# Kernel tuning notes

Measured on AMD Instinct MI355X. Metric: run time of the kernel, lower is better.

The kernel has to match this reference:

```python
import jax, jax.numpy as jnp
import numpy as np

K = 9
VOCAB = 7
DIM = 512
LOW = 256  # downsampled bottleneck dim
N_LAYERS = 2
EPS = 1e-5


def _inorm(x, g, b):
    # InstanceNorm1d over length axis (biased var), x: (N, C, K)
    m = jnp.mean(x, axis=-1, keepdims=True)
    v = jnp.mean((x - m) ** 2, axis=-1, keepdims=True)
    return g[None, :, None] * (x - m) * jax.lax.rsqrt(v + EPS) + b[None, :, None]


def _conv5_same(x, w, b):
    # x: (N, C, K), w: (O, C, 5), dilation 1, padding 'same' -> pad 2
    y = jax.lax.conv_general_dilated(
        x, w, window_strides=(1,), padding=[(2, 2)],
        dimension_numbers=('NCH', 'OIH', 'NCH'))
    return y + b[None, :, None]


def _bytenet_layer(x, p):
    (g1, b1, g2, b2, g3, b3, w1, c1b, w2, c2b, w3, c3b) = p
    h = jax.nn.gelu(_inorm(x, g1, b1), approximate=False)
    h = jnp.einsum('nck,oc->nok', h, w1) + c1b[None, :, None]      # 1x1 conv 512->256
    h = jax.nn.gelu(_inorm(h, g2, b2), approximate=False)
    h = _conv5_same(h, w2, c2b)                                     # k=5 conv 256->256
    h = jax.nn.gelu(_inorm(h, g3, b3), approximate=False)
    h = jnp.einsum('nck,oc->nok', h, w3) + c3b[None, :, None]      # 1x1 conv 256->512
    return h + x  # dropout is identity in eval


def setup_inputs() -> dict:
    key = jax.random.key(0)
    ks = jax.random.split(key, 16)
    x = jax.random.randint(ks[0], (8, 2048), 0, VOCAB)
    emb = jax.random.normal(ks[1], (VOCAB, DIM), jnp.float32) * 0.02
    emb = emb.at[6].set(0.0)  # padding_idx=6
    d = {
        'x': x,
        'emb': emb,
        'ln1_w': jnp.ones((N_LAYERS, DIM)), 'ln1_b': jnp.zeros((N_LAYERS, DIM)),
        'ln2_w': jnp.ones((N_LAYERS, LOW)), 'ln2_b': jnp.zeros((N_LAYERS, LOW)),
        'ln3_w': jnp.ones((N_LAYERS, LOW)), 'ln3_b': jnp.zeros((N_LAYERS, LOW)),
        'c1_w': jax.random.normal(ks[2], (N_LAYERS, LOW, DIM), jnp.float32) * 0.02,
        'c1_b': jnp.zeros((N_LAYERS, LOW)),
        'c2_w': jax.random.normal(ks[3], (N_LAYERS, LOW, LOW, 5), jnp.float32) * 0.02,
        'c2_b': jnp.zeros((N_LAYERS, LOW)),
        'c3_w': jax.random.normal(ks[4], (N_LAYERS, DIM, LOW), jnp.float32) * 0.02,
        'c3_b': jnp.zeros((N_LAYERS, DIM)),
        'out_w': jax.random.normal(ks[5], (VOCAB, DIM * K), jnp.float32) * 0.02,
        'out_b': jnp.zeros((VOCAB,)),
    }
    return d


def reference(x, emb, ln1_w, ln1_b, ln2_w, ln2_b, ln3_w, ln3_b,
              c1_w, c1_b, c2_w, c2_b, c3_w, c3_b, out_w, out_b):
    B, L = x.shape
    W = L - K + 1
    e = emb[x]                                        # (B, L, D)
    idx = jnp.arange(W)[:, None] + jnp.arange(K)      # (W, K)
    win = e[:, idx, :]                                # (B, W, K, D)
    h = win.transpose(0, 1, 3, 2).reshape(B * W, DIM, K)  # (N, D, K)
    for i in range(N_LAYERS):
        p = (ln1_w[i], ln1_b[i], ln2_w[i], ln2_b[i], ln3_w[i], ln3_b[i],
             c1_w[i], c1_b[i], c2_w[i], c2_b[i], c3_w[i], c3_b[i])
        h = _bytenet_layer(h, p)
    pred = h.reshape(B * W, DIM * K) @ out_w.T + out_b
    return pred.reshape(B, W, VOCAB)
```

## Files before the change

### kernel.cpp

```cpp
#include <hip/hip_runtime.h>

typedef __attribute__((ext_vector_type(8))) short bfv8;
typedef __attribute__((ext_vector_type(4))) float f32x4;
typedef __attribute__((ext_vector_type(4))) unsigned short usv4;

typedef __attribute__((address_space(1))) const void gvoid;
typedef __attribute__((address_space(3))) void lvoid;
__device__ __forceinline__ void gload16(const void* g, void* l) {
  __builtin_amdgcn_global_load_lds((gvoid*)g, (lvoid*)l, 16, 0, 0);
}

__device__ __forceinline__ float bf2f(unsigned short u) {
  union { unsigned int i; float f; } c; c.i = ((unsigned int)u) << 16; return c.f;
}
__device__ __forceinline__ unsigned short f2bf(float f) {
  union { float f; unsigned int i; } c; c.f = f;
  unsigned int r = c.i + 0x7FFFu + ((c.i >> 16) & 1u);
  return (unsigned short)(r >> 16);
}
__device__ __forceinline__ float gelu_(float x) {
  float z2 = 1.5957691216057308f * x * __builtin_fmaf(0.044715f, x * x, 1.0f);
  float e = __expf(z2);
  float t = __builtin_amdgcn_rcpf(e + 1.0f);
  return x - x * t;
}
__device__ __forceinline__ int div9(int col) {
  return (int)(__umulhi((unsigned)col, 954437177u) >> 1);
}

#define CHP 132
#define CHP2 66

__global__ void k_prep(const float* c1w, const float* c2w, const float* c3w,
                       const float* outw, unsigned short* W1b, unsigned short* W2t,
                       unsigned short* W3b, float* OWt) {
  int i = blockIdx.x * 256 + threadIdx.x;
  if (i < 262144) { W1b[i] = f2bf(c1w[i]); return; }
  i -= 262144;
  if (i < 655360) {
    int ii = i & 255, o = (i >> 8) & 255, rest = i >> 16;
    int t = rest % 5, l = rest / 5;
    W2t[i] = f2bf(c2w[(((l * 256 + o) << 8) + ii) * 5 + t]);
    return;
  }
  i -= 655360;
  if (i < 262144) { W3b[i] = f2bf(c3w[i]); return; }
  i -= 262144;
  if (i < 32256) {
    int c = i & 511, rk = i >> 9;
    int r = rk / 9, k = rk - 9 * r;
    OWt[i] = outw[r * 4608 + c * 9 + k];
  }
}

__global__ void k_x0(const int* x, const float* emb, unsigned short* X, int n0) {
  int idx = blockIdx.x * 256 + threadIdx.x;
  int c4 = idx & 127, nl = idx >> 7;
  int gn = n0 + nl, b = gn >> 11, w = gn & 2047;
  unsigned short* dst = X + (size_t)(12 + nl * 12) * 512 + (c4 << 2);
  const int* xb = x + (b << 11);
  #pragma unroll
  for (int k = 0; k < 9; k++) {
    int t = w + k; if (t > 2047) t = 2047;
    const float* e = emb + xb[t] * 512 + (c4 << 2);
    float4 ev = *(const float4*)e;
    usv4 pk;
    pk[0] = f2bf(ev.x); pk[1] = f2bf(ev.y);
    pk[2] = f2bf(ev.z); pk[3] = f2bf(ev.w);
    *(usv4*)(dst + k * 512) = pk;
  }
}

__global__ void k_zpad(unsigned short* AL) {
  int i = threadIdx.x;
  for (; i < 12 * 256; i += 256) AL[i] = 0;
}

template <int MODE>
__global__ __launch_bounds__(512, 2) void k_gemm(
    const unsigned short* __restrict__ Aw, const unsigned short* __restrict__ Bsrc,
    const float* __restrict__ n1w, const float* __restrict__ n1b,
    const float* __restrict__ gw, const float* __restrict__ gb,
    unsigned short* __restrict__ Out, int nkc) {
  __shared__ __align__(16) unsigned short smem[69632];
  unsigned short* sE = smem;

  const int KROW = (MODE == 0) ? 512 : 256;
  const int KSTEPS = (MODE == 1) ? 20 : 8;
  int tid = threadIdx.x, wv = tid >> 6, ln = tid & 63;
  int lr = ln >> 3, lu = ln & 7;
  int swz = (lu ^ lr) << 3;
  int w0 = blockIdx.x << 5;
  int col0 = blockIdx.x * 288;

  int brow[5];
  #pragma unroll
  for (int s = 0; s < 5; s++) {
    int colg = col0 + (s << 6) + (wv << 3) + lr;
    if (colg >= nkc) colg = nkc - 1;
    brow[s] = colg + 3 * div9(colg) + 12;
  }

  f32x4 acc[4][9];
  #pragma unroll
  for (int i = 0; i < 4; i++)
    #pragma unroll
    for (int j = 0; j < 9; j++) acc[i][j] = (f32x4){0.f, 0.f, 0.f, 0.f};

  auto stage = [&](int buf, int ks) {
    int kb, dlt; const unsigned short* Ab;
    if (MODE == 1) {
      int t = ks % 5; kb = (ks / 5) << 6; dlt = t - 2; Ab = Aw + t * 65536;
    } else { kb = ks << 6; dlt = 0; Ab = Aw; }
    unsigned short* cA = smem + buf * 16384;
    unsigned short* cB = smem + 32768 + buf * 18432;
    #pragma unroll
    for (int p = 0; p < 4; p++) {
      int m = (p << 6) + (wv << 3) + lr;
      gload16(Ab + (size_t)m * KROW + kb + swz, cA + (p << 12) + (wv << 9));
    }
    #pragma unroll
    for (int s = 0; s < 4; s++)
      gload16(Bsrc + (size_t)(brow[s] + dlt) * KROW + kb + swz,
              cB + (s << 12) + (wv << 9));
    if (wv < 4)
      gload16(Bsrc + (size_t)(brow[4] + dlt) * KROW + kb + swz,
              cB + (4 << 12) + (wv << 9));
  };

  stage(0, 0);
  __syncthreads();

  int cur = 0;
  for (int ks = 0; ks < KSTEPS; ks++) {
    unsigned short* cA = smem + cur * 16384;
    unsigned short* cB = smem + 32768 + cur * 18432;

    if (MODE == 0) {
      int cg = tid & 15, win = tid >> 4;
      int u = cg >> 1, sub = (cg & 1) << 3;
      int gch = (ks << 6) + (cg << 2);
      float v[9][4], s1[4] = {0.f, 0.f, 0.f, 0.f};
      #pragma unroll
      for (int k = 0; k < 9; k++) {
        int cl = win * 9 + k;
        usv4 rv = *(const usv4*)((char*)cB + cl * 128 + ((u ^ (cl & 7)) << 4) + sub);
        #pragma unroll
        for (int j = 0; j < 4; j++) { v[k][j] = bf2f(rv[j]); s1[j] += v[k][j]; }
      }
      float mn[4], rr[4], gg[4], bo[4];
      #pragma unroll
      for (int j = 0; j < 4; j++) {
        mn[j] = s1[j] * (1.0f / 9.0f);
        float q = 0.f;
        #pragma unroll
        for (int k = 0; k < 9; k++) { float d = v[k][j] - mn[j]; q += d * d; }
        rr[j] = rsqrtf(q * (1.0f / 9.0f) + 1e-5f);
        gg[j] = n1w[gch + j]; bo[j] = n1b[gch + j];
      }
      #pragma unroll
      for (int k = 0; k < 9; k++) {
        int cl = win * 9 + k;
        usv4 pk;
        #pragma unroll
        for (int j = 0; j < 4; j++)
          pk[j] = f2bf(gelu_(gg[j] * (v[k][j] - mn[j]) * rr[j] + bo[j]));
        *(usv4*)((char*)cB + cl * 128 + ((u ^ (cl & 7)) << 4) + sub) = pk;
      }
      __syncthreads();
    }

    if (ks + 1 < KSTEPS) stage(cur ^ 1, ks + 1);

    int l16 = ln & 15, loct = ln >> 4;
    int wm = wv >> 1, wn = wv & 1;
    #pragma unroll
    for (int kk = 0; kk < 2; kk++) {
      int kbyte = (kk << 6) + (loct << 4);
      bfv8 af[4], bf_[9];
      #pragma unroll
      for (int mi = 0; mi < 4; mi++) {
        int row = (wm << 6) + (mi << 4) + l16;
        af[mi] = *(const bfv8*)((const char*)cA + row * 128 + (kbyte ^ ((row & 7) << 4)));
      }
      #pragma unroll
      for (int ni = 0; ni < 9; ni++) {
        int row = wn * 144 + (ni << 4) + l16;
        bf_[ni] = *(const bfv8*)((const char*)cB + row * 128 + (kbyte ^ ((row & 7) << 4)));
      }
      #pragma unroll
      for (int mi = 0; mi < 4; mi++)
        #pragma unroll
        for (int ni = 0; ni < 9; ni++)
          acc[mi][ni] = __builtin_amdgcn_mfma_f32_16x16x32_bf16(
              af[mi], bf_[ni], acc[mi][ni], 0, 0, 0);
    }
    __syncthreads();
    cur ^= 1;
  }

  int l16 = ln & 15, loct = ln >> 4;
  #pragma unroll
  for (int R = 0; R < 2; R++) {
    if (R) __syncthreads();
    if ((wv >> 2) == R) {
      int chh = (((wv >> 1) & 1) << 6) + (loct << 2);
      int colb = (wv & 1) * 144 + l16;
      #pragma unroll
      for (int mi = 0; mi < 4; mi++) {
        #pragma unroll
        for (int ni = 0; ni < 9; ni++) {
          usv4 pk;
          #pragma unroll
          for (int q = 0; q < 4; q++) pk[q] = f2bf(acc[mi][ni][q]);
          *(usv4*)(sE + (colb + (ni << 4)) * CHP + chh + (mi << 4)) = pk;
        }
      }
    }
    __syncthreads();
    #pragma unroll
    for (int tt = 0; tt < 2; tt++) {
      int t = tid + tt * 512;
      int c4 = t & 31, win = t >> 5;
      int chl = (R << 7) + (c4 << 2);
      const unsigned short* sb = sE + (win * 9) * CHP + (c4 << 2);
      size_t ob = (size_t)(12 + (size_t)(w0 + win) * 12) * 256 + chl;
      float s1[4] = {0.f, 0.f, 0.f, 0.f}, s2[4] = {0.f, 0.f, 0.f, 0.f};
      #pragma unroll
      for (int k = 0; k < 9; k++) {
        usv4 rv = *(const usv4*)(sb + k * CHP);
        #pragma unroll
        for (int j = 0; j < 4; j++) {
          float f = bf2f(rv[j]);
          s1[j] += f; s2[j] = __builtin_fmaf(f, f, s2[j]);
        }
      }
      float mn[4], rr[4], gg[4], bo[4];
      #pragma unroll
      for (int j = 0; j < 4; j++) {
        mn[j] = s1[j] * (1.0f / 9.0f);
        float var = s2[j] * (1.0f / 9.0f) - mn[j] * mn[j];
        rr[j] = rsqrtf(var + 1e-5f);
        gg[j] = gw[chl + j]; bo[j] = gb[chl + j];
      }
      #pragma unroll
      for (int k = 0; k < 9; k++) {
        usv4 rv = *(const usv4*)(sb + k * CHP);
        usv4 pk;
        #pragma unroll
        for (int j = 0; j < 4; j++)
          pk[j] = f2bf(gelu_(gg[j] * (bf2f(rv[j]) - mn[j]) * rr[j] + bo[j]));
        *(usv4*)(Out + ob + k * 256) = pk;
      }
      if (MODE == 0) {
        usv4 z = (usv4){0, 0, 0, 0};
        *(usv4*)(Out + ob + 9 * 256) = z;
        *(usv4*)(Out + ob + 10 * 256) = z;
        *(usv4*)(Out + ob + 11 * 256) = z;
      }
    }
  }
}

__global__ __launch_bounds__(256, 2) void k_gemm2(
    const unsigned short* __restrict__ Aw, const unsigned short* __restrict__ Bsrc,
    const float* __restrict__ cbias, unsigned short* __restrict__ Out, int nkc) {
  __shared__ __align__(16) unsigned short smem[34816];
  unsigned short* sE = smem;

  const int KROW = 256, KSTEPS = 4;
  int tid = threadIdx.x, wv = tid >> 6, ln = tid & 63;
  int lr = ln >> 3, lu = ln & 7;
  int swz = (lu ^ lr) << 3;
  int m0 = (int)blockIdx.y << 7;
  int w0 = blockIdx.x << 4;
  int col0 = blockIdx.x * 144;

  int brow[5];
  #pragma unroll
  for (int s = 0; s < 5; s++) {
    int cl = (s < 4) ? ((s << 5) + (wv << 3) + lr) : (128 + (wv << 3) + lr);
    int colg = col0 + cl;
    if (colg >= nkc) colg = nkc - 1;
    brow[s] = colg + 3 * div9(colg) + 12;
  }
  const unsigned short* A0 = Aw + (size_t)m0 * KROW;

  f32x4 acc[2][9];
  #pragma unroll
  for (int i = 0; i < 2; i++)
    #pragma unroll
    for (int j = 0; j < 9; j++) acc[i][j] = (f32x4){0.f, 0.f, 0.f, 0.f};

  auto stage = [&](int buf, int ks) {
    int kb = ks << 6;
    unsigned short* cA = smem + buf * 8192;
    unsigned short* cB = smem + 16384 + buf * 9216;
    #pragma unroll
    for (int p = 0; p < 4; p++) {
      int m = (p << 5) + (wv << 3) + lr;
      gload16(A0 + (size_t)m * KROW + kb + swz, cA + ((p << 5) + (wv << 3)) * 64);
    }
    #pragma unroll
    for (int s = 0; s < 4; s++)
      gload16(Bsrc + (size_t)brow[s] * KROW + kb + swz,
              cB + ((s << 5) + (wv << 3)) * 64);
    if (wv < 2)
      gload16(Bsrc + (size_t)brow[4] * KROW + kb + swz,
              cB + (128 + (wv << 3)) * 64);
  };

  stage(0, 0);
  __syncthreads();

  int cur = 0;
  for (int ks = 0; ks < KSTEPS; ks++) {
    unsigned short* cA = smem + cur * 8192;
    unsigned short* cB = smem + 16384 + cur * 9216;
    if (ks + 1 < KSTEPS) stage(cur ^ 1, ks + 1);

    int l16 = ln & 15, loct = ln >> 4;
    #pragma unroll
    for (int kk = 0; kk < 2; kk++) {
      int kbyte = (kk << 6) + (loct << 4);
      bfv8 af[2], bf_[9];
      #pragma unroll
      for (int mi = 0; mi < 2; mi++) {
        int row = (wv << 5) + (mi << 4) + l16;
        af[mi] = *(const bfv8*)((const char*)cA + row * 128 + (kbyte ^ ((row & 7) << 4)));
      }
      #pragma unroll
      for (int ni = 0; ni < 9; ni++) {
        int row = (ni << 4) + l16;
        bf_[ni] = *(const bfv8*)((const char*)cB + row * 128 + (kbyte ^ ((row & 7) << 4)));
      }
      #pragma unroll
      for (int mi = 0; mi < 2; mi++)
        #pragma unroll
        for (int ni = 0; ni < 9; ni++)
          acc[mi][ni] = __builtin_amdgcn_mfma_f32_16x16x32_bf16(
              af[mi], bf_[ni], acc[mi][ni], 0, 0, 0);
    }
    __syncthreads();
    cur ^= 1;
  }

  int l16 = ln & 15, loct = ln >> 4;
  int c4 = tid & 15, win = tid >> 4;
  #pragma unroll
  for (int R = 0; R < 2; R++) {
    if (R) __syncthreads();
    if ((wv >> 1) == R) {
      int chh = ((wv & 1) << 5) + (loct << 2);
      #pragma unroll
      for (int mi = 0; mi < 2; mi++) {
        #pragma unroll
        for (int ni = 0; ni < 9; ni++) {
          usv4 pk;
          #pragma unroll
          for (int q = 0; q < 4; q++) pk[q] = f2bf(acc[mi][ni][q]);
          *(usv4*)(sE + ((ni << 4) + l16) * CHP2 + chh + (mi << 4)) = pk;
        }
      }
    }
    __syncthreads();
    {
      int chg = m0 + (R << 6) + (c4 << 2);
      const unsigned short* sb = sE + (win * 9) * CHP2 + (c4 << 2);
      size_t ob = (size_t)(12 + (size_t)(w0 + win) * 12) * 512 + chg;
      float cb[4];
      #pragma unroll
      for (int j = 0; j < 4; j++) cb[j] = cbias[chg + j];
      #pragma unroll
      for (int k = 0; k < 9; k++) {
        usv4 rv = *(const usv4*)(sb + k * CHP2);
        usv4 old = *(usv4*)(Out + ob + k * 512);
        usv4 pk;
        #pragma unroll
        for (int j = 0; j < 4; j++)
          pk[j] = f2bf(bf2f(rv[j]) + cb[j] + bf2f(old[j]));
        *(usv4*)(Out + ob + k * 512) = pk;
      }
    }
  }
}

__global__ void k_out(const unsigned short* X, const float* OWt, const float* outb,
                      float* pred, int n0, int nc) {
  int gw = (blockIdx.x * 256 + threadIdx.x) >> 6;
  int ln = threadIdx.x & 63;
  if (gw >= nc) return;
  int gn = n0 + gw, b = gn >> 11, w = gn & 2047;
  if (w >= 2040) return;
  const unsigned short* xb = X + (size_t)(12 + gw * 12) * 512 + ln * 8;
  float a[7];
  #pragma unroll
  for (int r = 0; r < 7; r++) a[r] = 0.f;
  for (int k = 0; k < 9; k++) {
    bfv8 xv = *(const bfv8*)(xb + k * 512);
    float xf[8];
    #pragma unroll
    for (int j = 0; j < 8; j++) xf[j] = bf2f((unsigned short)xv[j]);
    #pragma unroll
    for (int r = 0; r < 7; r++) {
      const float* wp = OWt + (r * 9 + k) * 512 + ln * 8;
      float4 w0 = *(const float4*)(wp);
      float4 w1 = *(const float4*)(wp + 4);
      a[r] += xf[0] * w0.x + xf[1] * w0.y + xf[2] * w0.z + xf[3] * w0.w +
              xf[4] * w1.x + xf[5] * w1.y + xf[6] * w1.z + xf[7] * w1.w;
    }
  }
  #pragma unroll
  for (int r = 0; r < 7; r++)
    for (int off = 32; off; off >>= 1) a[r] += __shfl_down(a[r], off);
  if (ln == 0) {
    float* o = pred + (size_t)(b * 2040 + w) * 7;
    #pragma unroll
    for (int r = 0; r < 7; r++) o[r] = a[r] + outb[r];
  }
}

extern "C" void kernel_launch(void* const* d_in, const int* in_sizes, int n_in,
                              void* d_out, int out_size, void* d_ws, size_t ws_size,
                              hipStream_t stream) {
  const int*   x    = (const int*)d_in[0];
  const float* emb  = (const float*)d_in[1];
  const float* ln1w = (const float*)d_in[2];
  const float* ln1b = (const float*)d_in[3];
  const float* ln2w = (const float*)d_in[4];
  const float* ln2b = (const float*)d_in[5];
  const float* ln3w = (const float*)d_in[6];
  const float* ln3b = (const float*)d_in[7];
  const float* c1w  = (const float*)d_in[8];
  const float* c2w  = (const float*)d_in[10];
  const float* c3w  = (const float*)d_in[12];
  const float* c3b  = (const float*)d_in[13];
  const float* outw = (const float*)d_in[14];
  const float* outb = (const float*)d_in[15];
  float* pred = (float*)d_out;

  int nc = 8192;
  while (nc > 128 &&
         2488320ull + (unsigned long long)(nc + 1) * 24576ull > ws_size)
    nc >>= 1;
  int nkc = nc * 9;
  int tiles288 = nc >> 5;
  int tiles144 = nc >> 4;
  int nchunks = 16384 / nc;

  char* ws = (char*)d_ws;
  unsigned short* W1b = (unsigned short*)(ws);
  unsigned short* W2t = (unsigned short*)(ws + 524288);
  unsigned short* W3b = (unsigned short*)(ws + 1835008);
  float*          OWt = (float*)(ws + 2359296);
  char* act = ws + 2488320;
  size_t hiB = (size_t)(nc + 1) * 12288;
  size_t loB = (size_t)(nc + 1) * 6144;
  unsigned short* X   = (unsigned short*)(act);
  unsigned short* AL  = (unsigned short*)(act + hiB);
  unsigned short* AL2 = (unsigned short*)(act + hiB + loB);

  k_prep<<<(1211904 + 255) / 256, 256, 0, stream>>>(c1w, c2w, c3w, outw,
                                                    W1b, W2t, W3b, OWt);
  k_zpad<<<1, 256, 0, stream>>>(AL);

  for (int ch = 0; ch < nchunks; ch++) {
    int n0 = ch * nc;
    k_x0<<<nc / 2, 256, 0, stream>>>(x, emb, X, n0);
    for (int l = 0; l < 2; l++) {
      k_gemm<0><<<dim3(tiles288, 1), 512, 0, stream>>>(
          W1b + l * 131072, X, ln1w + l * 512, ln1b + l * 512,
          ln2w + l * 256, ln2b + l * 256, AL, nkc);
      k_gemm<1><<<dim3(tiles288, 1), 512, 0, stream>>>(
          W2t + l * 327680, AL, nullptr, nullptr,
          ln3w + l * 256, ln3b + l * 256, AL2, nkc);
      k_gemm2<<<dim3(tiles144, 4), 256, 0, stream>>>(
          W3b + l * 131072, AL2, c3b + l * 512, X, nkc);
    }
    k_out<<<nc / 4, 256, 0, stream>>>(X, OWt, outb, pred, n0, nc);
  }
}
```

Baseline: 790.2 us.

## Fuse 1x1 conv and k=5 conv into one kernel keeping intermediate in LDS

Merges the first 1x1 conv GEMM (with inorm+gelu) and the k=5 conv GEMM into a single kernel per 16-window tile. The 256-channel intermediate stays in shared memory with zero halo rows, so it is never written to or re-read from global memory, and the zero-pad kernel and the AL buffer are dropped. Weights for both GEMMs are now read straight from global memory into registers instead of being staged in LDS. Tiles shrink from 32 to 16 windows, so each weight fragment is reused less and weight traffic through L2 rises.

```diff
diff --git a/kernel.cpp b/kernel.cpp
--- a/kernel.cpp
+++ b/kernel.cpp
@@ -28,7 +28,6 @@
   return (int)(__umulhi((unsigned)col, 954437177u) >> 1);
 }
 
-#define CHP 132
 #define CHP2 66
 
 __global__ void k_prep(const float* c1w, const float* c2w, const float* c3w,
@@ -71,80 +70,60 @@
   }
 }
 
-__global__ void k_zpad(unsigned short* AL) {
-  int i = threadIdx.x;
-  for (; i < 12 * 256; i += 256) AL[i] = 0;
-}
-
-template <int MODE>
-__global__ __launch_bounds__(512, 2) void k_gemm(
-    const unsigned short* __restrict__ Aw, const unsigned short* __restrict__ Bsrc,
-    const float* __restrict__ n1w, const float* __restrict__ n1b,
-    const float* __restrict__ gw, const float* __restrict__ gb,
-    unsigned short* __restrict__ Out, int nkc) {
-  __shared__ __align__(16) unsigned short smem[69632];
-  unsigned short* sE = smem;
-
-  const int KROW = (MODE == 0) ? 512 : 256;
-  const int KSTEPS = (MODE == 1) ? 20 : 8;
+__global__ __launch_bounds__(512, 2) void k_fused01(
+    const unsigned short* __restrict__ W1, const unsigned short* __restrict__ W2,
+    const unsigned short* __restrict__ Xg, const float* __restrict__ n1w,
+    const float* __restrict__ n1b, const float* __restrict__ n2w,
+    const float* __restrict__ n2b, const float* __restrict__ n3w,
+    const float* __restrict__ n3b, unsigned short* __restrict__ AL2g) {
+  __shared__ __align__(16) unsigned short smem[74752];
+  char* const a1c = (char*)(smem + 24576);
+
   int tid = threadIdx.x, wv = tid >> 6, ln = tid & 63;
-  int lr = ln >> 3, lu = ln & 7;
-  int swz = (lu ^ lr) << 3;
-  int w0 = blockIdx.x << 5;
-  int col0 = blockIdx.x * 288;
-
-  int brow[5];
-  #pragma unroll
-  for (int s = 0; s < 5; s++) {
-    int colg = col0 + (s << 6) + (wv << 3) + lr;
-    if (colg >= nkc) colg = nkc - 1;
-    brow[s] = colg + 3 * div9(colg) + 12;
-  }
-
-  f32x4 acc[4][9];
+  int l16 = ln & 15, loct = ln >> 4;
+  int wm = wv >> 1, wn = wv & 1;
+  int w0 = blockIdx.x << 4;
+  int grow0 = 12 + w0 * 12;
+
+  if (tid < 128) {
+    ((usv4*)a1c)[tid] = (usv4){0, 0, 0, 0};
+    ((usv4*)(a1c + 194 * 512))[tid] = (usv4){0, 0, 0, 0};
+  }
+
+  f32x4 acc[4][6];
   #pragma unroll
   for (int i = 0; i < 4; i++)
     #pragma unroll
-    for (int j = 0; j < 9; j++) acc[i][j] = (f32x4){0.f, 0.f, 0.f, 0.f};
-
-  auto stage = [&](int buf, int ks) {
-    int kb, dlt; const unsigned short* Ab;
-    if (MODE == 1) {
-      int t = ks % 5; kb = (ks / 5) << 6; dlt = t - 2; Ab = Aw + t * 65536;
-    } else { kb = ks << 6; dlt = 0; Ab = Aw; }
-    unsigned short* cA = smem + buf * 16384;
-    unsigned short* cB = smem + 32768 + buf * 18432;
-    #pragma unroll
-    for (int p = 0; p < 4; p++) {
-      int m = (p << 6) + (wv << 3) + lr;
-      gload16(Ab + (size_t)m * KROW + kb + swz, cA + (p << 12) + (wv << 9));
-    }
-    #pragma unroll
-    for (int s = 0; s < 4; s++)
-      gload16(Bsrc + (size_t)(brow[s] + dlt) * KROW + kb + swz,
-              cB + (s << 12) + (wv << 9));
-    if (wv < 4)
-      gload16(Bsrc + (size_t)(brow[4] + dlt) * KROW + kb + swz,
-              cB + (4 << 12) + (wv << 9));
+    for (int j = 0; j < 6; j++) acc[i][j] = (f32x4){0.f, 0.f, 0.f, 0.f};
+
+  auto stageXS = [&](int buf, int ks) {
+    int kb = ks << 6;
+    unsigned short* dst = smem + buf * 12288;
+    #pragma unroll
+    for (int i = 0; i < 3; i++) {
+      int c = tid + (i << 9);
+      int row = c >> 3, u = c & 7;
+      gload16(Xg + (size_t)(grow0 + row) * 512 + kb + ((u ^ (row & 7)) << 3),
+              dst + c * 8);
+    }
   };
 
-  stage(0, 0);
+  stageXS(0, 0);
   __syncthreads();
 
   int cur = 0;
-  for (int ks = 0; ks < KSTEPS; ks++) {
-    unsigned short* cA = smem + cur * 16384;
-    unsigned short* cB = smem + 32768 + cur * 18432;
-
-    if (MODE == 0) {
+  for (int ks = 0; ks < 8; ks++) {
+    char* xb = (char*)(smem + cur * 12288);
+
+    if (tid < 256) {
       int cg = tid & 15, win = tid >> 4;
-      int u = cg >> 1, sub = (cg & 1) << 3;
+      int chb = cg << 3;
       int gch = (ks << 6) + (cg << 2);
       float v[9][4], s1[4] = {0.f, 0.f, 0.f, 0.f};
       #pragma unroll
       for (int k = 0; k < 9; k++) {
-        int cl = win * 9 + k;
-        usv4 rv = *(const usv4*)((char*)cB + cl * 128 + ((u ^ (cl & 7)) << 4) + sub);
+        int row = win * 12 + k;
+        usv4 rv = *(const usv4*)(xb + row * 128 + (chb ^ ((row & 7) << 4)));
         #pragma unroll
         for (int j = 0; j < 4; j++) { v[k][j] = bf2f(rv[j]); s1[j] += v[k][j]; }
       }
@@ -160,38 +139,42 @@
       }
       #pragma unroll
       for (int k = 0; k < 9; k++) {
-        int cl = win * 9 + k;
+        int row = win * 12 + k;
         usv4 pk;
         #pragma unroll
         for (int j = 0; j < 4; j++)
           pk[j] = f2bf(gelu_(gg[j] * (v[k][j] - mn[j]) * rr[j] + bo[j]));
-        *(usv4*)((char*)cB + cl * 128 + ((u ^ (cl & 7)) << 4) + sub) = pk;
-      }
-      __syncthreads();
-    }
-
-    if (ks + 1 < KSTEPS) stage(cur ^ 1, ks + 1);
-
-    int l16 = ln & 15, loct = ln >> 4;
-    int wm = wv >> 1, wn = wv & 1;
+        *(usv4*)(xb + row * 128 + (chb ^ ((row & 7) << 4))) = pk;
+      }
+      usv4 z = (usv4){0, 0, 0, 0};
+      #pragma unroll
+      for (int k = 9; k < 12; k++) {
+        int row = win * 12 + k;
+        *(usv4*)(xb + row * 128 + (chb ^ ((row & 7) << 4))) = z;
+      }
+    }
+    __syncthreads();
+
+    if (ks + 1 < 8) stageXS(cur ^ 1, ks + 1);
+
+    int kb = ks << 6;
     #pragma unroll
     for (int kk = 0; kk < 2; kk++) {
       int kbyte = (kk << 6) + (loct << 4);
-      bfv8 af[4], bf_[9];
-      #pragma unroll
-      for (int mi = 0; mi < 4; mi++) {
-        int row = (wm << 6) + (mi << 4) + l16;
-        af[mi] = *(const bfv8*)((const char*)cA + row * 128 + (kbyte ^ ((row & 7) << 4)));
-      }
-      #pragma unroll
-      for (int ni = 0; ni < 9; ni++) {
-        int row = wn * 144 + (ni << 4) + l16;
-        bf_[ni] = *(const bfv8*)((const char*)cB + row * 128 + (kbyte ^ ((row & 7) << 4)));
-      }
+      bfv8 af[4], bf_[6];
       #pragma unroll
       for (int mi = 0; mi < 4; mi++)
-        #pragma unroll
-        for (int ni = 0; ni < 9; ni++)
+        af[mi] = *(const bfv8*)(W1 + (size_t)((wm << 6) + (mi << 4) + l16) * 512 +
+                                kb + (kk << 5) + (loct << 3));
+      #pragma unroll
+      for (int ni = 0; ni < 6; ni++) {
+        int row = wn * 96 + (ni << 4) + l16;
+        bf_[ni] = *(const bfv8*)(xb + row * 128 + (kbyte ^ ((row & 7) << 4)));
+      }
+      #pragma unroll
+      for (int mi = 0; mi < 4; mi++)
+        #pragma unroll
+        for (int ni = 0; ni < 6; ni++)
           acc[mi][ni] = __builtin_amdgcn_mfma_f32_16x16x32_bf16(
               af[mi], bf_[ni], acc[mi][ni], 0, 0, 0);
     }
@@ -199,65 +182,131 @@
     cur ^= 1;
   }
 
-  int l16 = ln & 15, loct = ln >> 4;
-  #pragma unroll
-  for (int R = 0; R < 2; R++) {
-    if (R) __syncthreads();
-    if ((wv >> 2) == R) {
-      int chh = (((wv >> 1) & 1) << 6) + (loct << 2);
-      int colb = (wv & 1) * 144 + l16;
-      #pragma unroll
-      for (int mi = 0; mi < 4; mi++) {
-        #pragma unroll
-        for (int ni = 0; ni < 9; ni++) {
-          usv4 pk;
-          #pragma unroll
-          for (int q = 0; q < 4; q++) pk[q] = f2bf(acc[mi][ni][q]);
-          *(usv4*)(sE + (colb + (ni << 4)) * CHP + chh + (mi << 4)) = pk;
-        }
-      }
-    }
-    __syncthreads();
-    #pragma unroll
-    for (int tt = 0; tt < 2; tt++) {
-      int t = tid + tt * 512;
-      int c4 = t & 31, win = t >> 5;
-      int chl = (R << 7) + (c4 << 2);
-      const unsigned short* sb = sE + (win * 9) * CHP + (c4 << 2);
-      size_t ob = (size_t)(12 + (size_t)(w0 + win) * 12) * 256 + chl;
-      float s1[4] = {0.f, 0.f, 0.f, 0.f}, s2[4] = {0.f, 0.f, 0.f, 0.f};
-      #pragma unroll
-      for (int k = 0; k < 9; k++) {
-        usv4 rv = *(const usv4*)(sb + k * CHP);
-        #pragma unroll
-        for (int j = 0; j < 4; j++) {
-          float f = bf2f(rv[j]);
-          s1[j] += f; s2[j] = __builtin_fmaf(f, f, s2[j]);
-        }
-      }
-      float mn[4], rr[4], gg[4], bo[4];
-      #pragma unroll
-      for (int j = 0; j < 4; j++) {
-        mn[j] = s1[j] * (1.0f / 9.0f);
-        float var = s2[j] * (1.0f / 9.0f) - mn[j] * mn[j];
-        rr[j] = rsqrtf(var + 1e-5f);
-        gg[j] = gw[chl + j]; bo[j] = gb[chl + j];
-      }
-      #pragma unroll
-      for (int k = 0; k < 9; k++) {
-        usv4 rv = *(const usv4*)(sb + k * CHP);
-        usv4 pk;
-        #pragma unroll
-        for (int j = 0; j < 4; j++)
-          pk[j] = f2bf(gelu_(gg[j] * (bf2f(rv[j]) - mn[j]) * rr[j] + bo[j]));
-        *(usv4*)(Out + ob + k * 256) = pk;
-      }
-      if (MODE == 0) {
-        usv4 z = (usv4){0, 0, 0, 0};
-        *(usv4*)(Out + ob + 9 * 256) = z;
-        *(usv4*)(Out + ob + 10 * 256) = z;
-        *(usv4*)(Out + ob + 11 * 256) = z;
-      }
+  #pragma unroll
+  for (int mi = 0; mi < 4; mi++) {
+    int chb = (wm << 7) + (mi << 5) + (loct << 3);
+    #pragma unroll
+    for (int ni = 0; ni < 6; ni++) {
+      int row = 2 + wn * 96 + (ni << 4) + l16;
+      usv4 pk;
+      #pragma unroll
+      for (int q = 0; q < 4; q++) pk[q] = f2bf(acc[mi][ni][q]);
+      *(usv4*)(a1c + row * 512 + (chb ^ ((row & 7) << 4))) = pk;
+    }
+  }
+  __syncthreads();
+
+  #pragma unroll
+  for (int i = 0; i < 2; i++) {
+    int t = tid + (i << 9);
+    int cg = t & 63, win = (t >> 6) & 15;
+    int chb = cg << 3, gch = cg << 2;
+    float v[9][4], s1[4] = {0.f, 0.f, 0.f, 0.f};
+    #pragma unroll
+    for (int k = 0; k < 9; k++) {
+      int row = 2 + win * 12 + k;
+      usv4 rv = *(const usv4*)(a1c + row * 512 + (chb ^ ((row & 7) << 4)));
+      #pragma unroll
+      for (int j = 0; j < 4; j++) { v[k][j] = bf2f(rv[j]); s1[j] += v[k][j]; }
+    }
+    float mn[4], rr[4], gg[4], bo[4];
+    #pragma unroll
+    for (int j = 0; j < 4; j++) {
+      mn[j] = s1[j] * (1.0f / 9.0f);
+      float q = 0.f;
+      #pragma unroll
+      for (int k = 0; k < 9; k++) { float d = v[k][j] - mn[j]; q += d * d; }
+      rr[j] = rsqrtf(q * (1.0f / 9.0f) + 1e-5f);
+      gg[j] = n2w[gch + j]; bo[j] = n2b[gch + j];
+    }
+    #pragma unroll
+    for (int k = 0; k < 9; k++) {
+      int row = 2 + win * 12 + k;
+      usv4 pk;
+      #pragma unroll
+      for (int j = 0; j < 4; j++)
+        pk[j] = f2bf(gelu_(gg[j] * (v[k][j] - mn[j]) * rr[j] + bo[j]));
+      *(usv4*)(a1c + row * 512 + (chb ^ ((row & 7) << 4))) = pk;
+    }
+  }
+  __syncthreads();
+
+  #pragma unroll
+  for (int i = 0; i < 4; i++)
+    #pragma unroll
+    for (int j = 0; j < 6; j++) acc[i][j] = (f32x4){0.f, 0.f, 0.f, 0.f};
+
+  for (int ks = 0; ks < 20; ks++) {
+    int t = ks >> 2, kb = (ks & 3) << 6, dlt = t - 2;
+    const unsigned short* W2b = W2 + t * 65536;
+    #pragma unroll
+    for (int kk = 0; kk < 2; kk++) {
+      int kbyte = (kb << 1) + (kk << 6) + (loct << 4);
+      bfv8 af[4], bf_[6];
+      #pragma unroll
+      for (int mi = 0; mi < 4; mi++)
+        af[mi] = *(const bfv8*)(W2b + (size_t)((wm << 6) + (mi << 4) + l16) * 256 +
+                                kb + (kk << 5) + (loct << 3));
+      #pragma unroll
+      for (int ni = 0; ni < 6; ni++) {
+        int row = 2 + wn * 96 + (ni << 4) + l16 + dlt;
+        bf_[ni] = *(const bfv8*)(a1c + row * 512 + (kbyte ^ ((row & 7) << 4)));
+      }
+      #pragma unroll
+      for (int mi = 0; mi < 4; mi++)
+        #pragma unroll
+        for (int ni = 0; ni < 6; ni++)
+          acc[mi][ni] = __builtin_amdgcn_mfma_f32_16x16x32_bf16(
+              af[mi], bf_[ni], acc[mi][ni], 0, 0, 0);
+    }
+  }
+  __syncthreads();
+
+  #pragma unroll
+  for (int mi = 0; mi < 4; mi++) {
+    int chb = (wm << 7) + (mi << 5) + (loct << 3);
+    #pragma unroll
+    for (int ni = 0; ni < 6; ni++) {
+      int row = 2 + wn * 96 + (ni << 4) + l16;
+      usv4 pk;
+      #pragma unroll
+      for (int q = 0; q < 4; q++) pk[q] = f2bf(acc[mi][ni][q]);
+      *(usv4*)(a1c + row * 512 + (chb ^ ((row & 7) << 4))) = pk;
+    }
+  }
+  __syncthreads();
+
+  #pragma unroll
+  for (int i = 0; i < 2; i++) {
+    int t = tid + (i << 9);
+    int cg = t & 63, win = (t >> 6) & 15;
+    int chb = cg << 3, gch = cg << 2;
+    float v[9][4], s1[4] = {0.f, 0.f, 0.f, 0.f};
+    #pragma unroll
+    for (int k = 0; k < 9; k++) {
+      int row = 2 + win * 12 + k;
+      usv4 rv = *(const usv4*)(a1c + row * 512 + (chb ^ ((row & 7) << 4)));
+      #pragma unroll
+      for (int j = 0; j < 4; j++) { v[k][j] = bf2f(rv[j]); s1[j] += v[k][j]; }
+    }
+    float mn[4], rr[4], gg[4], bo[4];
+    #pragma unroll
+    for (int j = 0; j < 4; j++) {
+      mn[j] = s1[j] * (1.0f / 9.0f);
+      float q = 0.f;
+      #pragma unroll
+      for (int k = 0; k < 9; k++) { float d = v[k][j] - mn[j]; q += d * d; }
+      rr[j] = rsqrtf(q * (1.0f / 9.0f) + 1e-5f);
+      gg[j] = n3w[gch + j]; bo[j] = n3b[gch + j];
+    }
+    size_t gb = (size_t)(12 + (size_t)(w0 + win) * 12) * 256 + (cg << 2);
+    #pragma unroll
+    for (int k = 0; k < 9; k++) {
+      usv4 pk;
+      #pragma unroll
+      for (int j = 0; j < 4; j++)
+        pk[j] = f2bf(gelu_(gg[j] * (v[k][j] - mn[j]) * rr[j] + bo[j]));
+      *(usv4*)(AL2g + gb + k * 256) = pk;
     }
   }
 }
@@ -441,11 +490,10 @@
 
   int nc = 8192;
   while (nc > 128 &&
-         2488320ull + (unsigned long long)(nc + 1) * 24576ull > ws_size)
+         2488320ull + (unsigned long long)(nc + 1) * 18432ull > ws_size)
     nc >>= 1;
   int nkc = nc * 9;
-  int tiles288 = nc >> 5;
-  int tiles144 = nc >> 4;
+  int tiles16 = nc >> 4;
   int nchunks = 16384 / nc;
 
   char* ws = (char*)d_ws;
@@ -455,26 +503,21 @@
   float*          OWt = (float*)(ws + 2359296);
   char* act = ws + 2488320;
   size_t hiB = (size_t)(nc + 1) * 12288;
-  size_t loB = (size_t)(nc + 1) * 6144;
   unsigned short* X   = (unsigned short*)(act);
-  unsigned short* AL  = (unsigned short*)(act + hiB);
-  unsigned short* AL2 = (unsigned short*)(act + hiB + loB);
+  unsigned short* AL2 = (unsigned short*)(act + hiB);
 
   k_prep<<<(1211904 + 255) / 256, 256, 0, stream>>>(c1w, c2w, c3w, outw,
                                                     W1b, W2t, W3b, OWt);
-  k_zpad<<<1, 256, 0, stream>>>(AL);
 
   for (int ch = 0; ch < nchunks; ch++) {
     int n0 = ch * nc;
     k_x0<<<nc / 2, 256, 0, stream>>>(x, emb, X, n0);
     for (int l = 0; l < 2; l++) {
-      k_gemm<0><<<dim3(tiles288, 1), 512, 0, stream>>>(
-          W1b + l * 131072, X, ln1w + l * 512, ln1b + l * 512,
-          ln2w + l * 256, ln2b + l * 256, AL, nkc);
-      k_gemm<1><<<dim3(tiles288, 1), 512, 0, stream>>>(
-          W2t + l * 327680, AL, nullptr, nullptr,
-          ln3w + l * 256, ln3b + l * 256, AL2, nkc);
-      k_gemm2<<<dim3(tiles144, 4), 256, 0, stream>>>(
+      k_fused01<<<tiles16, 512, 0, stream>>>(
+          W1b + l * 131072, W2t + l * 327680, X,
+          ln1w + l * 512, ln1b + l * 512, ln2w + l * 256, ln2b + l * 256,
+          ln3w + l * 256, ln3b + l * 256, AL2);
+      k_gemm2<<<dim3(tiles16, 4), 256, 0, stream>>>(
           W3b + l * 131072, AL2, c3b + l * 512, X, nkc);
     }
     k_out<<<nc / 4, 256, 0, stream>>>(X, OWt, outb, pred, n0, nc);
```

Measured after the change: 1.045 ms. 1.32x slower.
